# Optimization experiments

Measured on AMD Instinct MI355X. Metric: run time of the kernel, lower is better.

The kernel has to match this reference:

```python
import jax, jax.numpy as jnp
import numpy as np

B, L, WIN = 65536, 240, 24
EMB_SZS = [(367, 20), (7, 4), (24, 8)]
N_CONT = 16
H1, H2, OUT_SZ = 512, 256, 24
N_EMB = sum(nf for _, nf in EMB_SZS)
NUM_WAVE = 6 * (WIN // 2) + 6 * (WIN // 4)  # 108


def pool_matrix(lin, w):
    # PyTorch AdaptiveAvgPool1d: bin i averages x[floor(i*lin/w) : ceil((i+1)*lin/w)]
    P = np.zeros((lin, w), np.float32)
    for i in range(w):
        s = (i * lin) // w
        e = -((-(i + 1) * lin) // w)
        P[s:e, i] = 1.0 / (e - s)
    return jnp.asarray(P)


def conv1(x, w, dil):
    # single-channel 1D cross-correlation, no bias; x: [B, Lin], w: [ks]
    ks = w.shape[0]
    lout = x.shape[-1] - dil * (ks - 1)
    return sum(w[k] * x[:, k * dil:k * dil + lout] for k in range(ks))


def branch(xw, wa, wb):
    # conv(ks, dil=1) -> adaptive_avg_pool(12) -> leaky_relu(0.1), then same with dil=2 -> pool(6)
    ca = conv1(xw, wa, 1)                                   # [B, L-ks+1]
    fa = jax.nn.leaky_relu(ca @ pool_matrix(ca.shape[-1], WIN // 2), 0.1)  # [B,12]
    cb = conv1(fa, wb, 2)                                   # [B, 12-2*(ks-1)]
    fb = jax.nn.leaky_relu(cb @ pool_matrix(cb.shape[-1], WIN // 4), 0.1)  # [B,6]
    return fa, fb


def setup_inputs() -> dict:
    key = jax.random.key(0)
    ks_list = list(range(1, 7))
    keys = jax.random.split(key, 32)
    d = {}
    d['x_window'] = jax.random.normal(keys[0], (B, 1, L), jnp.float32)
    cats = [jax.random.randint(jax.random.fold_in(keys[1], i), (B,), 0, ni)
            for i, (ni, _) in enumerate(EMB_SZS)]
    d['x_cat'] = jnp.stack(cats, axis=1).astype(jnp.int64)
    d['x_cont'] = jax.random.normal(keys[2], (B, N_CONT), jnp.float32)
    for i, ks in enumerate(ks_list):
        d[f'wk{ks}a'] = jax.random.normal(keys[3 + 2 * i], (ks,), jnp.float32) * 0.5
        d[f'wk{ks}b'] = jax.random.normal(keys[4 + 2 * i], (ks,), jnp.float32) * 0.5
    for i, (ni, nf) in enumerate(EMB_SZS):
        d[f'E{i}'] = jax.random.normal(keys[16 + i], (ni, nf), jnp.float32) * 0.01
    d['bn_g'] = jnp.ones((N_CONT,), jnp.float32)
    d['bn_b'] = jnp.zeros((N_CONT,), jnp.float32)
    n_in = N_EMB + N_CONT
    d['W1'] = jax.random.normal(keys[20], (n_in, H1), jnp.float32) * (1.0 / np.sqrt(n_in))
    d['b1'] = jnp.zeros((H1,), jnp.float32)
    d['W2'] = jax.random.normal(keys[21], (H1, H2), jnp.float32) * (1.0 / np.sqrt(H1))
    d['b2'] = jnp.zeros((H2,), jnp.float32)
    d['Wlin'] = jax.random.normal(keys[22], (NUM_WAVE + H2, OUT_SZ), jnp.float32) * (1.0 / np.sqrt(NUM_WAVE + H2))
    return d


def reference(x_window, x_cat, x_cont,
              wk1a, wk1b, wk2a, wk2b, wk3a, wk3b, wk4a, wk4b, wk5a, wk5b, wk6a, wk6b,
              E0, E1, E2, bn_g, bn_b, W1, b1, W2, b2, Wlin):
    xw = x_window[:, 0, :]  # [B, L]
    feats = []
    for wa, wb in [(wk1a, wk1b), (wk2a, wk2b), (wk3a, wk3b),
                   (wk4a, wk4b), (wk5a, wk5b), (wk6a, wk6b)]:
        fa, fb = branch(xw, wa, wb)
        feats += [fa, fb]
    ffc = jnp.concatenate(feats, axis=1)  # [B, 108]
    # embeddings
    emb = jnp.concatenate([E0[x_cat[:, 0]], E1[x_cat[:, 1]], E2[x_cat[:, 2]]], axis=1)  # [B, 32]
    # BatchNorm1d on continuous features (training-mode batch stats, eps=1e-5)
    m = jnp.mean(x_cont, axis=0)
    v = jnp.var(x_cont, axis=0)
    xc = (x_cont - m) / jnp.sqrt(v + 1e-5) * bn_g + bn_b
    x = jnp.concatenate([emb, xc], axis=1)  # [B, 48]
    x = jax.nn.relu(x @ W1 + b1)
    x = jax.nn.relu(x @ W2 + b2)  # [B, 256]
    fc = jnp.concatenate([ffc, x], axis=1)  # [B, 364]
    return fc @ Wlin  # [B, 24]
```

## Files before the change

kernel.cpp:

```cpp
#include <hip/hip_runtime.h>

typedef __bf16 bf16x8 __attribute__((ext_vector_type(8)));
typedef float  f32x4  __attribute__((ext_vector_type(4)));
typedef unsigned short ushort_t;

#define B_TOTAL 65536

__device__ __forceinline__ ushort_t f2bf(float f) {
  unsigned u = __builtin_bit_cast(unsigned, f);
  u += 0x7fffu + ((u >> 16) & 1u);
  return (ushort_t)(u >> 16);
}
__device__ __forceinline__ unsigned pk2(float lo, float hi) {
  unsigned r;
  asm("v_cvt_pk_bf16_f32 %0, %1, %2" : "=v"(r) : "v"(lo), "v"(hi));
  return r;
}
__device__ __forceinline__ float lrelu(float v) { return v >= 0.f ? v : 0.1f * v; }
__device__ __forceinline__ bf16x8 ld_frag(const ushort_t* p8) {
  return __builtin_bit_cast(bf16x8, *(const uint4*)p8);
}
__device__ __forceinline__ bf16x8 ld_tile(const ushort_t* base, int tile, int lane) {
  return __builtin_bit_cast(bf16x8,
      *(const uint4*)((const char*)base + tile * 1024 + lane * 16));
}
__device__ __forceinline__ char* frag_addr(ushort_t* base, int k, int s15, int st) {
  int kb = k >> 5, g = (k >> 3) & 3, i = k & 7;
  return (char*)base + ((kb * 2 + st) * 64 + s15 + g * 16) * 16 + i * 2;
}
__device__ __forceinline__ f32x4 mfma16(bf16x8 a, bf16x8 b, f32x4 c) {
  return __builtin_amdgcn_mfma_f32_16x16x32_bf16(a, b, c, 0, 0, 0);
}

__global__ __launch_bounds__(256) void bn_partial(const float* __restrict__ xc,
                                                  float* __restrict__ ws) {
  __shared__ float red[512];
  const int t = threadIdx.x;
  const int c = t & 15, g = t >> 4;
  const int r0 = blockIdx.x * 256;
  float s = 0.f, q = 0.f;
  for (int i = 0; i < 16; ++i) {
    float v = xc[(size_t)(r0 + g + i * 16) * 16 + c];
    s += v; q += v * v;
  }
  red[t] = s; red[256 + t] = q;
  __syncthreads();
  if (t < 16) {
    float ss = 0.f, qq = 0.f;
    for (int gg = 0; gg < 16; ++gg) { ss += red[gg * 16 + t]; qq += red[256 + gg * 16 + t]; }
    ws[blockIdx.x * 32 + t] = ss;
    ws[blockIdx.x * 32 + 16 + t] = qq;
  }
}

__global__ __launch_bounds__(256) void bn_final(const float* __restrict__ ws_in,
                                                float* __restrict__ ws_out,
                                                const float* __restrict__ g_,
                                                const float* __restrict__ b_) {
  __shared__ float red[512];
  const int t = threadIdx.x;
  const int c = t & 15, g = t >> 4;
  float s = 0.f, q = 0.f;
  for (int i = 0; i < 16; ++i) {
    int blk = g * 16 + i;
    s += ws_in[blk * 32 + c];
    q += ws_in[blk * 32 + 16 + c];
  }
  red[t] = s; red[256 + t] = q;
  __syncthreads();
  if (t < 16) {
    float ss = 0.f, qq = 0.f;
    for (int gg = 0; gg < 16; ++gg) { ss += red[gg * 16 + t]; qq += red[256 + gg * 16 + t]; }
    float mean  = ss / (float)B_TOTAL;
    float var   = qq / (float)B_TOTAL - mean * mean;
    float scale = g_[t] / sqrtf(var + 1e-5f);
    ws_out[8192 + t]      = scale;
    ws_out[8192 + 16 + t] = b_[t] - mean * scale;
  }
}

__global__ __launch_bounds__(256) void pack_weights(const float* __restrict__ W1,
                                                    const float* __restrict__ W2,
                                                    const float* __restrict__ Wl,
                                                    ushort_t* __restrict__ w1p,
                                                    ushort_t* __restrict__ w2p,
                                                    ushort_t* __restrict__ wlp) {
  int u = blockIdx.x * 256 + threadIdx.x;
  if (u < 32768) {
    int i = u & 7, lane = (u >> 3) & 63, kb = u >> 14;
    int k = kb * 32 + ((lane >> 4) << 3) + i;
    int n = (((u >> 9) & 31) << 4) + (lane & 15);
    w1p[u] = f2bf(k < 48 ? W1[k * 512 + n] : 0.f);
  } else if (u < 32768 + 131072) {
    int v = u - 32768;
    int i = v & 7, lane = (v >> 3) & 63, kb = v >> 13;
    int k = kb * 32 + ((lane >> 4) << 3) + i;
    int n = (((v >> 9) & 15) << 4) + (lane & 15);
    w2p[v] = f2bf(W2[k * 256 + n]);
  } else if (u < 32768 + 131072 + 12288) {
    int v = u - (32768 + 131072);
    int i = v & 7, lane = (v >> 3) & 63, kb = v >> 10;
    int k = kb * 32 + ((lane >> 4) << 3) + i;
    int n = (((v >> 9) & 1) << 4) + (lane & 15);
    float val = 0.f;
    if (n < 24) {
      if (k < 108)       val = Wl[k * 24 + n];
      else if (k >= 128) val = Wl[(k - 20) * 24 + n];
    }
    wlp[v] = f2bf(val);
  }
}

struct WkPtrs { const float* wk[12]; };

__global__ __launch_bounds__(256) void pack_conv(WkPtrs wp,
                                                 ushort_t* __restrict__ Apack,
                                                 ushort_t* __restrict__ Bpack) {
  int u = blockIdx.x * 256 + threadIdx.x;
  if (u < 20480) {
    int i = u & 7, lane = (u >> 3) & 63;
    int knt = u >> 9;
    int kb = knt / 5, nt = knt % 5;
    int k = kb * 32 + ((lane >> 4) << 3) + i;
    int n = nt * 16 + (lane & 15);
    float val = 0.f;
    if (n < 72 && k < 240) {
      int br = n / 12, ii = n - br * 12, ks = br + 1, lin = 240 - br;
      int si = ii * lin / 12, ei = ((ii + 1) * lin + 11) / 12;
      const float* wa = wp.wk[2 * br];
      float acc = 0.f;
      for (int kk = 0; kk < ks; ++kk) {
        int j = k - kk;
        if (j >= si && j < ei) acc += wa[kk];
      }
      val = acc / (float)(ei - si);
    }
    Apack[u] = f2bf(val);
  } else if (u < 20480 + 6144) {
    int v = u - 20480;
    int i = v & 7, lane = (v >> 3) & 63;
    int knt = v >> 9;
    int kb = knt / 3, nt = knt % 3;
    int kcol = kb * 32 + ((lane >> 4) << 3) + i;
    int n = nt * 16 + (lane & 15);
    float val = 0.f;
    if (n < 36 && kcol < 108) {
      int brk = kcol / 18, ii = kcol - brk * 18;
      int brn = n / 6, j = n - brn * 6;
      if (brk == brn && ii < 12) {
        int ks = brn + 1, lcb = 12 - 2 * brn;
        int sj = j * lcb / 6, ej = ((j + 1) * lcb + 5) / 6;
        const float* wb = wp.wk[2 * brn + 1];
        float acc = 0.f;
        for (int kk = 0; kk < ks; ++kk) {
          int q = ii - 2 * kk;
          if (q >= sj && q < ej) acc += wb[kk];
        }
        val = acc / (float)(ej - sj);
      }
    }
    Bpack[v] = f2bf(val);
  }
}

struct FusedParams {
  const float* xw;
  const int*   xcat;
  const float* xcont;
  const float* E0; const float* E1; const float* E2;
  const float* b1; const float* b2;
  const ushort_t* Apack; const ushort_t* Bpack;
  const ushort_t* w1p; const ushort_t* w2p; const ushort_t* wlp;
  const float* stats;
  float*       out;
};

__global__ __launch_bounds__(512, 6) void fused_kernel(FusedParams p) {
  __shared__ __align__(16) char smem[45056];
  ushort_t* s_xw  = (ushort_t*)smem;
  ushort_t* s_h1  = (ushort_t*)smem;
  ushort_t* s_h2  = (ushort_t*)smem;
  ushort_t* s_cf  = (ushort_t*)(smem + 32768);
  ushort_t* s_x48 = (ushort_t*)(smem + 40960);

  const int t    = threadIdx.x;
  const int lane = t & 63;
  const int w    = t >> 6;
  const int quad = lane >> 4;
  const int s15  = lane & 15;
  const int s0   = blockIdx.x * 32;
  const f32x4 fzero = {0.f, 0.f, 0.f, 0.f};

  ((uint4*)s_cf)[t] = uint4{0, 0, 0, 0};
  if (t < 64) {
    *(uint4*)((char*)s_xw + (14 + (t >> 5)) * 1024 + 512 + (t & 31) * 16) = uint4{0, 0, 0, 0};
  } else if (t < 128) {
    int tt = t - 64;
    *(uint4*)((char*)s_x48 + (2 + (tt >> 5)) * 1024 + 512 + (tt & 31) * 16) = uint4{0, 0, 0, 0};
  }
  for (int u = t; u < 32 * 60; u += 512) {
    int s = u / 60, m4 = u - s * 60;
    float4 v = *(const float4*)(p.xw + (size_t)(s0 + s) * 240 + 4 * m4);
    uint2 pkv; pkv.x = pk2(v.x, v.y); pkv.y = pk2(v.z, v.w);
    int kb = m4 >> 3, g = (m4 >> 1) & 3;
    *(uint2*)((char*)s_xw + ((kb * 2 + (s >> 4)) * 64 + (s & 15) + g * 16) * 16
              + (m4 & 1) * 8) = pkv;
  }
  for (int u = t; u < 32 * 48; u += 512) {
    int s = u / 48, c = u - s * 48, gs = s0 + s;
    float v;
    if (c < 20)      v = p.E0[(size_t)p.xcat[gs * 3 + 0] * 20 + c];
    else if (c < 24) v = p.E1[(size_t)p.xcat[gs * 3 + 1] * 4 + (c - 20)];
    else if (c < 32) v = p.E2[(size_t)p.xcat[gs * 3 + 2] * 8 + (c - 24)];
    else { int cc = c - 32; v = p.xcont[(size_t)gs * 16 + cc] * p.stats[cc] + p.stats[16 + cc]; }
    *(ushort_t*)frag_addr(s_x48, c, s & 15, s >> 4) = f2bf(v);
  }
  __syncthreads();

  auto do0a = [&](int nt, int st) {
    f32x4 acc = fzero;
    #pragma unroll
    for (int kb = 0; kb < 8; ++kb) {
      bf16x8 a = ld_frag(p.Apack + (size_t)((kb * 5 + nt) * 64 + lane) * 8);
      bf16x8 b = ld_tile(s_xw, kb * 2 + st, lane);
      acc = mfma16(a, b, acc);
    }
    int n0 = nt * 16 + quad * 4;
    int br = n0 / 12;
    int col0 = n0 + 6 * br;
    *(unsigned*)frag_addr(s_cf, col0, s15, st)     = pk2(lrelu(acc[0]), lrelu(acc[1]));
    *(unsigned*)frag_addr(s_cf, col0 + 2, s15, st) = pk2(lrelu(acc[2]), lrelu(acc[3]));
  };
  do0a(w % 5, w / 5);
  if (w < 2) do0a(w + 3, 1);
  __syncthreads();

  const int nt2 = w * 2;
  uint4 pa[2][2];
  #pragma unroll
  for (int q = 0; q < 2; ++q) {
    pa[q][0] = *(const uint4*)(p.w2p + (size_t)((q * 16 + nt2 + 0) * 64 + lane) * 8);
    pa[q][1] = *(const uint4*)(p.w2p + (size_t)((q * 16 + nt2 + 1) * 64 + lane) * 8);
  }

  const int ntB = w % 3, stB = w / 3;
  f32x4 accB = fzero;
  if (w < 6) {
    #pragma unroll
    for (int kb = 0; kb < 4; ++kb) {
      bf16x8 a = ld_frag(p.Bpack + (size_t)((kb * 3 + ntB) * 64 + lane) * 8);
      bf16x8 b = ld_tile(s_cf, kb * 2 + stB, lane);
      accB = mfma16(a, b, accB);
    }
  }

  {
    bf16x8 bx[2][2];
    #pragma unroll
    for (int st = 0; st < 2; ++st)
      #pragma unroll
      for (int kb = 0; kb < 2; ++kb)
        bx[st][kb] = ld_tile(s_x48, kb * 2 + st, lane);
    #pragma unroll
    for (int j = 0; j < 4; ++j) {
      int nt = w * 4 + j;
      bf16x8 a0 = ld_frag(p.w1p + (size_t)((0 * 32 + nt) * 64 + lane) * 8);
      bf16x8 a1 = ld_frag(p.w1p + (size_t)((1 * 32 + nt) * 64 + lane) * 8);
      f32x4 acc[2];
      #pragma unroll
      for (int st = 0; st < 2; ++st) {
        acc[st] = mfma16(a0, bx[st][0], fzero);
        acc[st] = mfma16(a1, bx[st][1], acc[st]);
      }
      int n0 = nt * 16 + quad * 4;
      float4 bb = *(const float4*)(p.b1 + n0);
      int kb1 = nt >> 1;
      int g   = (nt * 2 + (quad >> 1)) & 3;
      #pragma unroll
      for (int st = 0; st < 2; ++st) {
        float v0 = fmaxf(acc[st][0] + bb.x, 0.f);
        float v1 = fmaxf(acc[st][1] + bb.y, 0.f);
        float v2 = fmaxf(acc[st][2] + bb.z, 0.f);
        float v3 = fmaxf(acc[st][3] + bb.w, 0.f);
        uint2 pkv; pkv.x = pk2(v0, v1); pkv.y = pk2(v2, v3);
        *(uint2*)((char*)s_h1 + ((kb1 * 2 + st) * 64 + s15 + g * 16) * 16
                  + (quad & 1) * 8) = pkv;
      }
    }
  }
  __syncthreads();

  if (w < 6) {
    int n0 = ntB * 16 + quad * 4;
    if (n0 < 36) {
      int br0 = n0 / 6, c0 = n0 + 12 * (br0 + 1);
      int n2 = n0 + 2, br2 = n2 / 6, c2 = n2 + 12 * (br2 + 1);
      *(unsigned*)frag_addr(s_cf, c0, s15, stB) = pk2(lrelu(accB[0]), lrelu(accB[1]));
      *(unsigned*)frag_addr(s_cf, c2, s15, stB) = pk2(lrelu(accB[2]), lrelu(accB[3]));
    }
  }

  f32x4 acc2[2][2];
  #pragma unroll
  for (int jm = 0; jm < 2; ++jm) { acc2[jm][0] = fzero; acc2[jm][1] = fzero; }
  #pragma unroll
  for (int kb = 0; kb < 16; ++kb) {
    bf16x8 a0 = __builtin_bit_cast(bf16x8, pa[kb & 1][0]);
    bf16x8 a1 = __builtin_bit_cast(bf16x8, pa[kb & 1][1]);
    if (kb < 14) {
      pa[kb & 1][0] = *(const uint4*)(p.w2p + (size_t)(((kb + 2) * 16 + nt2 + 0) * 64 + lane) * 8);
      pa[kb & 1][1] = *(const uint4*)(p.w2p + (size_t)(((kb + 2) * 16 + nt2 + 1) * 64 + lane) * 8);
    }
    #pragma unroll
    for (int st = 0; st < 2; ++st) {
      bf16x8 b = ld_tile(s_h1, kb * 2 + st, lane);
      acc2[0][st] = mfma16(a0, b, acc2[0][st]);
      acc2[1][st] = mfma16(a1, b, acc2[1][st]);
    }
  }
  __syncthreads();

  #pragma unroll
  for (int jm = 0; jm < 2; ++jm) {
    int n0 = (nt2 + jm) * 16 + quad * 4;
    float4 bb = *(const float4*)(p.b2 + n0);
    int kbh = (nt2 + jm) >> 1;
    int g   = ((nt2 + jm) * 2 + (quad >> 1)) & 3;
    #pragma unroll
    for (int st = 0; st < 2; ++st) {
      float v0 = fmaxf(acc2[jm][st][0] + bb.x, 0.f);
      float v1 = fmaxf(acc2[jm][st][1] + bb.y, 0.f);
      float v2 = fmaxf(acc2[jm][st][2] + bb.z, 0.f);
      float v3 = fmaxf(acc2[jm][st][3] + bb.w, 0.f);
      uint2 pkv; pkv.x = pk2(v0, v1); pkv.y = pk2(v2, v3);
      *(uint2*)((char*)s_h2 + ((kbh * 2 + st) * 64 + s15 + g * 16) * 16
                + (quad & 1) * 8) = pkv;
    }
  }
  __syncthreads();

  if (w < 4) {
    const int st = w & 1, nt = w >> 1;
    f32x4 acc = fzero;
    #pragma unroll
    for (int kb = 0; kb < 12; ++kb) {
      bf16x8 a = ld_frag(p.wlp + (size_t)((kb * 2 + nt) * 64 + lane) * 8);
      bf16x8 b = (kb < 4) ? ld_tile(s_cf, kb * 2 + st, lane)
                          : ld_tile(s_h2, (kb - 4) * 2 + st, lane);
      acc = mfma16(a, b, acc);
    }
    int n0 = nt * 16 + quad * 4;
    if (n0 < 24) {
      int sg = s0 + st * 16 + s15;
      *(float2*)(p.out + (size_t)sg * 24 + n0)     = make_float2(acc[0], acc[1]);
      *(float2*)(p.out + (size_t)sg * 24 + n0 + 2) = make_float2(acc[2], acc[3]);
    }
  }
}

extern "C" void kernel_launch(void* const* d_in, const int* in_sizes, int n_in,
                              void* d_out, int out_size, void* d_ws, size_t ws_size,
                              hipStream_t stream) {
  const float* xcont = (const float*)d_in[2];
  float* ws  = (float*)d_ws;
  char*  wsb = (char*)d_ws;
  ushort_t* w1p   = (ushort_t*)(wsb + 36864);
  ushort_t* w2p   = (ushort_t*)(wsb + 102400);
  ushort_t* wlp   = (ushort_t*)(wsb + 364544);
  ushort_t* Apack = (ushort_t*)(wsb + 389120);
  ushort_t* Bpack = (ushort_t*)(wsb + 430080);

  WkPtrs wp;
  for (int i = 0; i < 12; ++i) wp.wk[i] = (const float*)d_in[3 + i];
  pack_conv<<<104, 256, 0, stream>>>(wp, Apack, Bpack);
  bn_partial<<<256, 256, 0, stream>>>(xcont, ws);
  bn_final<<<1, 256, 0, stream>>>(ws, ws, (const float*)d_in[18], (const float*)d_in[19]);
  pack_weights<<<688, 256, 0, stream>>>((const float*)d_in[20], (const float*)d_in[22],
                                        (const float*)d_in[24], w1p, w2p, wlp);

  FusedParams p;
  p.xw    = (const float*)d_in[0];
  p.xcat  = (const int*)d_in[1];
  p.xcont = xcont;
  p.E0 = (const float*)d_in[15]; p.E1 = (const float*)d_in[16]; p.E2 = (const float*)d_in[17];
  p.b1 = (const float*)d_in[21]; p.b2 = (const float*)d_in[23];
  p.Apack = Apack; p.Bpack = Bpack;
  p.w1p = w1p; p.w2p = w2p; p.wlp = wlp;
  p.stats = ws + 8192;
  p.out = (float*)d_out;
  fused_kernel<<<B_TOTAL / 32, 512, 0, stream>>>(p);
}
```

Measured before the change: 68.64 us.

## Process 64 samples per block and split hidden-layer GEMMs into halves

Each block now handles 64 samples instead of 32. Every weight fragment loaded from global memory (W1, W2, conv packs, Wlin) therefore feeds four MFMA column tiles instead of two, which halves weight traffic per sample. To fit h1 for 64 samples in shared memory, GEMM1 and GEMM2 are split into two 256-wide halves that reuse the same buffer, with extra barriers between them. LDS grows to 56KB and the occupancy hint drops from 6 to 4 blocks, which reduces latency hiding.

```diff
diff --git a/kernel.cpp b/kernel.cpp
--- a/kernel.cpp
+++ b/kernel.cpp
@@ -24,9 +24,9 @@
   return __builtin_bit_cast(bf16x8,
       *(const uint4*)((const char*)base + tile * 1024 + lane * 16));
 }
-__device__ __forceinline__ char* frag_addr(ushort_t* base, int k, int s15, int st) {
+__device__ __forceinline__ char* frag_addr4(ushort_t* base, int k, int s15, int st) {
   int kb = k >> 5, g = (k >> 3) & 3, i = k & 7;
-  return (char*)base + ((kb * 2 + st) * 64 + s15 + g * 16) * 16 + i * 2;
+  return (char*)base + (((kb * 4 + st) * 64) + s15 + g * 16) * 16 + i * 2;
 }
 __device__ __forceinline__ f32x4 mfma16(bf16x8 a, bf16x8 b, f32x4 c) {
   return __builtin_amdgcn_mfma_f32_16x16x32_bf16(a, b, c, 0, 0, 0);
@@ -175,45 +175,46 @@
   float*       out;
 };
 
-__global__ __launch_bounds__(512, 6) void fused_kernel(FusedParams p) {
-  __shared__ __align__(16) char smem[45056];
+__global__ __launch_bounds__(512, 4) void fused_kernel(FusedParams p) {
+  __shared__ __align__(16) char smem[57344];
   ushort_t* s_xw  = (ushort_t*)smem;
   ushort_t* s_h1  = (ushort_t*)smem;
   ushort_t* s_h2  = (ushort_t*)smem;
   ushort_t* s_cf  = (ushort_t*)(smem + 32768);
-  ushort_t* s_x48 = (ushort_t*)(smem + 40960);
+  ushort_t* s_x48 = (ushort_t*)(smem + 49152);
 
   const int t    = threadIdx.x;
   const int lane = t & 63;
   const int w    = t >> 6;
   const int quad = lane >> 4;
   const int s15  = lane & 15;
-  const int s0   = blockIdx.x * 32;
+  const int s0   = blockIdx.x * 64;
   const f32x4 fzero = {0.f, 0.f, 0.f, 0.f};
 
   ((uint4*)s_cf)[t] = uint4{0, 0, 0, 0};
-  if (t < 64) {
-    *(uint4*)((char*)s_xw + (14 + (t >> 5)) * 1024 + 512 + (t & 31) * 16) = uint4{0, 0, 0, 0};
-  } else if (t < 128) {
-    int tt = t - 64;
-    *(uint4*)((char*)s_x48 + (2 + (tt >> 5)) * 1024 + 512 + (tt & 31) * 16) = uint4{0, 0, 0, 0};
-  }
-  for (int u = t; u < 32 * 60; u += 512) {
+  ((uint4*)s_cf)[t + 512] = uint4{0, 0, 0, 0};
+  if (t < 128) {
+    *(uint4*)((char*)s_xw + (28 + (t >> 5)) * 1024 + 512 + (t & 31) * 16) = uint4{0, 0, 0, 0};
+  } else if (t < 256) {
+    int tt = t - 128;
+    *(uint4*)((char*)s_x48 + (4 + (tt >> 5)) * 1024 + 512 + (tt & 31) * 16) = uint4{0, 0, 0, 0};
+  }
+  for (int u = t; u < 64 * 60; u += 512) {
     int s = u / 60, m4 = u - s * 60;
     float4 v = *(const float4*)(p.xw + (size_t)(s0 + s) * 240 + 4 * m4);
     uint2 pkv; pkv.x = pk2(v.x, v.y); pkv.y = pk2(v.z, v.w);
-    int kb = m4 >> 3, g = (m4 >> 1) & 3;
-    *(uint2*)((char*)s_xw + ((kb * 2 + (s >> 4)) * 64 + (s & 15) + g * 16) * 16
+    int tile = (m4 >> 3) * 4 + (s >> 4);
+    *(uint2*)((char*)s_xw + (tile * 64 + (s & 15) + ((m4 >> 1) & 3) * 16) * 16
               + (m4 & 1) * 8) = pkv;
   }
-  for (int u = t; u < 32 * 48; u += 512) {
+  for (int u = t; u < 64 * 48; u += 512) {
     int s = u / 48, c = u - s * 48, gs = s0 + s;
     float v;
     if (c < 20)      v = p.E0[(size_t)p.xcat[gs * 3 + 0] * 20 + c];
     else if (c < 24) v = p.E1[(size_t)p.xcat[gs * 3 + 1] * 4 + (c - 20)];
     else if (c < 32) v = p.E2[(size_t)p.xcat[gs * 3 + 2] * 8 + (c - 24)];
     else { int cc = c - 32; v = p.xcont[(size_t)gs * 16 + cc] * p.stats[cc] + p.stats[16 + cc]; }
-    *(ushort_t*)frag_addr(s_x48, c, s & 15, s >> 4) = f2bf(v);
+    *(ushort_t*)frag_addr4(s_x48, c, s & 15, s >> 4) = f2bf(v);
   }
   __syncthreads();
 
@@ -222,17 +223,18 @@
     #pragma unroll
     for (int kb = 0; kb < 8; ++kb) {
       bf16x8 a = ld_frag(p.Apack + (size_t)((kb * 5 + nt) * 64 + lane) * 8);
-      bf16x8 b = ld_tile(s_xw, kb * 2 + st, lane);
+      bf16x8 b = ld_tile(s_xw, kb * 4 + st, lane);
       acc = mfma16(a, b, acc);
     }
     int n0 = nt * 16 + quad * 4;
     int br = n0 / 12;
     int col0 = n0 + 6 * br;
-    *(unsigned*)frag_addr(s_cf, col0, s15, st)     = pk2(lrelu(acc[0]), lrelu(acc[1]));
-    *(unsigned*)frag_addr(s_cf, col0 + 2, s15, st) = pk2(lrelu(acc[2]), lrelu(acc[3]));
+    *(unsigned*)frag_addr4(s_cf, col0, s15, st)     = pk2(lrelu(acc[0]), lrelu(acc[1]));
+    *(unsigned*)frag_addr4(s_cf, col0 + 2, s15, st) = pk2(lrelu(acc[2]), lrelu(acc[3]));
   };
   do0a(w % 5, w / 5);
-  if (w < 2) do0a(w + 3, 1);
+  do0a((w + 8) % 5, (w + 8) / 5);
+  if (w < 4) do0a((w + 16) % 5, (w + 16) / 5);
   __syncthreads();
 
   const int nt2 = w * 2;
@@ -243,81 +245,101 @@
     pa[q][1] = *(const uint4*)(p.w2p + (size_t)((q * 16 + nt2 + 1) * 64 + lane) * 8);
   }
 
-  const int ntB = w % 3, stB = w / 3;
-  f32x4 accB = fzero;
-  if (w < 6) {
+  const int ntB0 = w % 3,       stB0 = w / 3;
+  const int ntB1 = (w + 8) % 3, stB1 = (w + 8) / 3;
+  f32x4 accB0 = fzero, accB1 = fzero;
+  #pragma unroll
+  for (int kb = 0; kb < 4; ++kb) {
+    bf16x8 a = ld_frag(p.Bpack + (size_t)((kb * 3 + ntB0) * 64 + lane) * 8);
+    bf16x8 b = ld_tile(s_cf, kb * 4 + stB0, lane);
+    accB0 = mfma16(a, b, accB0);
+  }
+  if (w < 4) {
     #pragma unroll
     for (int kb = 0; kb < 4; ++kb) {
-      bf16x8 a = ld_frag(p.Bpack + (size_t)((kb * 3 + ntB) * 64 + lane) * 8);
-      bf16x8 b = ld_tile(s_cf, kb * 2 + stB, lane);
-      accB = mfma16(a, b, accB);
-    }
-  }
-
-  {
-    bf16x8 bx[2][2];
-    #pragma unroll
-    for (int st = 0; st < 2; ++st)
+      bf16x8 a = ld_frag(p.Bpack + (size_t)((kb * 3 + ntB1) * 64 + lane) * 8);
+      bf16x8 b = ld_tile(s_cf, kb * 4 + stB1, lane);
+      accB1 = mfma16(a, b, accB1);
+    }
+  }
+
+  auto gemm1_half = [&](int h) {
+    #pragma unroll
+    for (int j = 0; j < 2; ++j) {
+      int ntp = w * 2 + j;
+      int gnt = h * 16 + ntp;
+      bf16x8 a0 = ld_frag(p.w1p + (size_t)((0 * 32 + gnt) * 64 + lane) * 8);
+      bf16x8 a1 = ld_frag(p.w1p + (size_t)((32 + gnt) * 64 + lane) * 8);
+      f32x4 acc[4];
       #pragma unroll
-      for (int kb = 0; kb < 2; ++kb)
-        bx[st][kb] = ld_tile(s_x48, kb * 2 + st, lane);
-    #pragma unroll
-    for (int j = 0; j < 4; ++j) {
-      int nt = w * 4 + j;
-      bf16x8 a0 = ld_frag(p.w1p + (size_t)((0 * 32 + nt) * 64 + lane) * 8);
-      bf16x8 a1 = ld_frag(p.w1p + (size_t)((1 * 32 + nt) * 64 + lane) * 8);
-      f32x4 acc[2];
+      for (int st = 0; st < 4; ++st) {
+        bf16x8 b0 = ld_tile(s_x48, 0 * 4 + st, lane);
+        bf16x8 b1 = ld_tile(s_x48, 1 * 4 + st, lane);
+        acc[st] = mfma16(a0, b0, fzero);
+        acc[st] = mfma16(a1, b1, acc[st]);
+      }
+      int n0l = ntp * 16 + quad * 4;
+      float4 bb = *(const float4*)(p.b1 + h * 256 + n0l);
+      int kb1 = ntp >> 1;
+      int g   = (ntp * 2 + (quad >> 1)) & 3;
       #pragma unroll
-      for (int st = 0; st < 2; ++st) {
-        acc[st] = mfma16(a0, bx[st][0], fzero);
-        acc[st] = mfma16(a1, bx[st][1], acc[st]);
-      }
-      int n0 = nt * 16 + quad * 4;
-      float4 bb = *(const float4*)(p.b1 + n0);
-      int kb1 = nt >> 1;
-      int g   = (nt * 2 + (quad >> 1)) & 3;
-      #pragma unroll
-      for (int st = 0; st < 2; ++st) {
+      for (int st = 0; st < 4; ++st) {
         float v0 = fmaxf(acc[st][0] + bb.x, 0.f);
         float v1 = fmaxf(acc[st][1] + bb.y, 0.f);
         float v2 = fmaxf(acc[st][2] + bb.z, 0.f);
         float v3 = fmaxf(acc[st][3] + bb.w, 0.f);
         uint2 pkv; pkv.x = pk2(v0, v1); pkv.y = pk2(v2, v3);
-        *(uint2*)((char*)s_h1 + ((kb1 * 2 + st) * 64 + s15 + g * 16) * 16
+        *(uint2*)((char*)s_h1 + ((kb1 * 4 + st) * 64 + s15 + g * 16) * 16
                   + (quad & 1) * 8) = pkv;
       }
     }
-  }
-  __syncthreads();
-
-  if (w < 6) {
-    int n0 = ntB * 16 + quad * 4;
+  };
+  gemm1_half(0);
+  __syncthreads();
+
+  auto wr0b = [&](f32x4 acc, int nt, int st) {
+    int n0 = nt * 16 + quad * 4;
     if (n0 < 36) {
       int br0 = n0 / 6, c0 = n0 + 12 * (br0 + 1);
       int n2 = n0 + 2, br2 = n2 / 6, c2 = n2 + 12 * (br2 + 1);
-      *(unsigned*)frag_addr(s_cf, c0, s15, stB) = pk2(lrelu(accB[0]), lrelu(accB[1]));
-      *(unsigned*)frag_addr(s_cf, c2, s15, stB) = pk2(lrelu(accB[2]), lrelu(accB[3]));
-    }
-  }
-
-  f32x4 acc2[2][2];
+      *(unsigned*)frag_addr4(s_cf, c0, s15, st) = pk2(lrelu(acc[0]), lrelu(acc[1]));
+      *(unsigned*)frag_addr4(s_cf, c2, s15, st) = pk2(lrelu(acc[2]), lrelu(acc[3]));
+    }
+  };
+  wr0b(accB0, ntB0, stB0);
+  if (w < 4) wr0b(accB1, ntB1, stB1);
+
+  f32x4 acc2[2][4];
   #pragma unroll
-  for (int jm = 0; jm < 2; ++jm) { acc2[jm][0] = fzero; acc2[jm][1] = fzero; }
-  #pragma unroll
-  for (int kb = 0; kb < 16; ++kb) {
-    bf16x8 a0 = __builtin_bit_cast(bf16x8, pa[kb & 1][0]);
-    bf16x8 a1 = __builtin_bit_cast(bf16x8, pa[kb & 1][1]);
-    if (kb < 14) {
-      pa[kb & 1][0] = *(const uint4*)(p.w2p + (size_t)(((kb + 2) * 16 + nt2 + 0) * 64 + lane) * 8);
-      pa[kb & 1][1] = *(const uint4*)(p.w2p + (size_t)(((kb + 2) * 16 + nt2 + 1) * 64 + lane) * 8);
-    }
-    #pragma unroll
-    for (int st = 0; st < 2; ++st) {
-      bf16x8 b = ld_tile(s_h1, kb * 2 + st, lane);
-      acc2[0][st] = mfma16(a0, b, acc2[0][st]);
-      acc2[1][st] = mfma16(a1, b, acc2[1][st]);
-    }
-  }
+  for (int jm = 0; jm < 2; ++jm)
+    #pragma unroll
+    for (int st = 0; st < 4; ++st) acc2[jm][st] = fzero;
+
+  auto gemm2_half = [&](int k0) {
+    #pragma unroll
+    for (int kk = 0; kk < 8; ++kk) {
+      int kb = k0 + kk;
+      bf16x8 a0 = __builtin_bit_cast(bf16x8, pa[kb & 1][0]);
+      bf16x8 a1 = __builtin_bit_cast(bf16x8, pa[kb & 1][1]);
+      if (kb + 2 < 16) {
+        pa[kb & 1][0] = *(const uint4*)(p.w2p + (size_t)(((kb + 2) * 16 + nt2 + 0) * 64 + lane) * 8);
+        pa[kb & 1][1] = *(const uint4*)(p.w2p + (size_t)(((kb + 2) * 16 + nt2 + 1) * 64 + lane) * 8);
+      }
+      #pragma unroll
+      for (int st = 0; st < 4; ++st) {
+        bf16x8 b = ld_tile(s_h1, kk * 4 + st, lane);
+        acc2[0][st] = mfma16(a0, b, acc2[0][st]);
+        acc2[1][st] = mfma16(a1, b, acc2[1][st]);
+      }
+    }
+  };
+  gemm2_half(0);
+  __syncthreads();
+
+  gemm1_half(1);
+  __syncthreads();
+
+  gemm2_half(8);
   __syncthreads();
 
   #pragma unroll
@@ -327,26 +349,26 @@
     int kbh = (nt2 + jm) >> 1;
     int g   = ((nt2 + jm) * 2 + (quad >> 1)) & 3;
     #pragma unroll
-    for (int st = 0; st < 2; ++st) {
+    for (int st = 0; st < 4; ++st) {
       float v0 = fmaxf(acc2[jm][st][0] + bb.x, 0.f);
       float v1 = fmaxf(acc2[jm][st][1] + bb.y, 0.f);
       float v2 = fmaxf(acc2[jm][st][2] + bb.z, 0.f);
       float v3 = fmaxf(acc2[jm][st][3] + bb.w, 0.f);
       uint2 pkv; pkv.x = pk2(v0, v1); pkv.y = pk2(v2, v3);
-      *(uint2*)((char*)s_h2 + ((kbh * 2 + st) * 64 + s15 + g * 16) * 16
+      *(uint2*)((char*)s_h2 + ((kbh * 4 + st) * 64 + s15 + g * 16) * 16
                 + (quad & 1) * 8) = pkv;
     }
   }
   __syncthreads();
 
-  if (w < 4) {
-    const int st = w & 1, nt = w >> 1;
+  {
+    const int st = w & 3, nt = w >> 2;
     f32x4 acc = fzero;
     #pragma unroll
     for (int kb = 0; kb < 12; ++kb) {
       bf16x8 a = ld_frag(p.wlp + (size_t)((kb * 2 + nt) * 64 + lane) * 8);
-      bf16x8 b = (kb < 4) ? ld_tile(s_cf, kb * 2 + st, lane)
-                          : ld_tile(s_h2, (kb - 4) * 2 + st, lane);
+      bf16x8 b = (kb < 4) ? ld_tile(s_cf, kb * 4 + st, lane)
+                          : ld_tile(s_h2, (kb - 4) * 4 + st, lane);
       acc = mfma16(a, b, acc);
     }
     int n0 = nt * 16 + quad * 4;
@@ -388,5 +410,5 @@
   p.w1p = w1p; p.w2p = w2p; p.wlp = wlp;
   p.stats = ws + 8192;
   p.out = (float*)d_out;
-  fused_kernel<<<B_TOTAL / 32, 512, 0, stream>>>(p);
-}
+  fused_kernel<<<B_TOTAL / 64, 512, 0, stream>>>(p);
+}
```

Result: faster. 65.67 us (-4.3%).
